# Kernel tuning notes

Measured on AMD Instinct MI355X. Metric: run time of the kernel, lower is better.

The kernel has to match this reference:

```python
import jax, jax.numpy as jnp
import numpy as np

T = 2048
D_MODEL = 4096
N_HEADS = 32
N_GROUPS = 8
HEAD_DIM = 128


def _rope_tables(tokens, head_dim, base=10000.0):
    inv_freq = 1.0 / (base ** (np.arange(0, head_dim, 2, dtype=np.float32) / head_dim))
    pos = np.arange(tokens, dtype=np.float32)
    freqs = np.einsum('t,d->td', pos, inv_freq)          # [T, D/2]
    emb = np.concatenate([freqs, freqs], axis=-1)         # [T, D]
    return jnp.asarray(np.cos(emb)), jnp.asarray(np.sin(emb))


def setup_inputs() -> dict:
    key = jax.random.key(0)
    k1, k2, k3 = jax.random.split(key, 3)
    x = jax.random.normal(k1, (T, D_MODEL), dtype=jnp.float32)
    w_qkv = jax.random.normal(k2, (D_MODEL, (N_HEADS + 2 * N_GROUPS) * HEAD_DIM), dtype=jnp.float32) * 0.02
    w_out = jax.random.normal(k3, (N_HEADS * HEAD_DIM, D_MODEL), dtype=jnp.float32) * 0.02
    cos, sin = _rope_tables(T, HEAD_DIM)
    mask = jnp.tril(jnp.ones((T, T), dtype=bool))  # causal: [suffix_tokens, total_tokens]
    return {"x": x, "w_qkv": w_qkv, "w_out": w_out, "cos": cos, "sin": sin, "mask": mask}


def _rotate_half(u):
    u1, u2 = jnp.split(u, 2, axis=-1)
    return jnp.concatenate([-u2, u1], axis=-1)


def _apply_rope(u, cos, sin):
    # u: [tokens, heads, head_dim]; cos/sin: [tokens, head_dim]
    c = cos[:, None, :]
    s = sin[:, None, :]
    return u * c + _rotate_half(u) * s


def reference(x, w_qkv, w_out, cos, sin, mask):
    group_dim = N_HEADS // N_GROUPS
    qkv = x @ w_qkv                                        # [T, (H+2G)*D]
    q, k, v = jnp.split(qkv, [N_HEADS * HEAD_DIM, (N_HEADS + N_GROUPS) * HEAD_DIM], axis=-1)
    q = q.reshape(T, N_HEADS, HEAD_DIM)
    k = k.reshape(T, N_GROUPS, HEAD_DIM)
    v = v.reshape(T, N_GROUPS, HEAD_DIM)
    q = _apply_rope(q, cos, sin)
    k = _apply_rope(k, cos, sin)
    # GQA: group queries -> [T, G, group_dim, D]
    qg = q.reshape(T, N_GROUPS, group_dim, HEAD_DIM)
    scale = 1.0 / jnp.sqrt(jnp.asarray(HEAD_DIM, dtype=q.dtype))
    scores = jnp.einsum('tghd,sgd->ghts', qg, k) * scale   # [G, gd, T, S]
    neg = jnp.asarray(jnp.finfo(scores.dtype).min, scores.dtype)
    scores = jnp.where(mask[None, None, :, :], scores, neg)
    probs = jax.nn.softmax(scores, axis=-1)
    out = jnp.einsum('ghts,sgd->tghd', probs, v)           # [T, G, gd, D]
    out = out.reshape(T, N_HEADS * HEAD_DIM)
    return out @ w_out                                     # [T, model_dim]
```

## Files before the change

kernel.cpp:

```cpp
#include <hip/hip_runtime.h>
#include <cstdint>
#include <cstddef>

#define TT   2048
#define DM   4096
#define NH   32
#define NG   8
#define HD   128
#define QKVN 6144
#define KOFF 4096
#define VOFF 5120

typedef __attribute__((ext_vector_type(8))) short bf16x8;
typedef __attribute__((ext_vector_type(4))) float f32x4;
typedef unsigned short u16;

__device__ __forceinline__ u16 f2b(float f) {
  unsigned u = __builtin_bit_cast(unsigned, f);
  u += 0x7fffu + ((u >> 16) & 1u);
  return (u16)(u >> 16);
}
__device__ __forceinline__ float b2f(u16 s) {
  unsigned u = ((unsigned)s) << 16;
  return __builtin_bit_cast(float, u);
}

__device__ __forceinline__ void gload_lds16(const void* g, void* l) {
  __builtin_amdgcn_global_load_lds(
      (const __attribute__((address_space(1))) unsigned int*)g,
      (__attribute__((address_space(3))) unsigned int*)l,
      16, 0, 0);
}

__global__ __launch_bounds__(256) void cvt_f32_bf16(
    const float* __restrict__ src, u16* __restrict__ dst, int n) {
  for (int i = (blockIdx.x * 256 + threadIdx.x) * 4; i < n; i += gridDim.x * 256 * 4) {
    float4 v = *(const float4*)(src + i);
    ushort4 o;
    o.x = f2b(v.x); o.y = f2b(v.y); o.z = f2b(v.z); o.w = f2b(v.w);
    *(ushort4*)(dst + i) = o;
  }
}

__global__ __launch_bounds__(256) void transpose_cvt(
    const float* __restrict__ src, u16* __restrict__ dst, int R, int C) {
  __shared__ u16 tile[64][66];
  const int rb = blockIdx.y * 64, cb = blockIdx.x * 64;
  const int tid = threadIdx.x;
#pragma unroll
  for (int it = 0; it < 16; ++it) {
    int idx = it * 256 + tid;
    int i = idx >> 6, j = idx & 63;
    tile[i][j] = f2b(src[(size_t)(rb + i) * C + cb + j]);
  }
  __syncthreads();
#pragma unroll
  for (int it = 0; it < 16; ++it) {
    int idx = it * 256 + tid;
    int j = idx >> 6, i = idx & 63;
    dst[(size_t)(cb + j) * R + rb + i] = tile[i][j];
  }
}

template <bool OUT_BF16>
__global__ __launch_bounds__(512) void gemm8p(
    const u16* __restrict__ A, const u16* __restrict__ Bt, void* __restrict__ Cout,
    int M, int N, int K, int nbx) {
  __shared__ __align__(16) u16 sA[2][128 * 64];
  __shared__ __align__(16) u16 sB[2][256 * 64];
  const int tid = threadIdx.x;
  const int wid = tid >> 6, lane = tid & 63;
  const int lane15 = lane & 15, laneh = lane >> 4;
  const int wm = wid >> 2, wn = wid & 3;
  const int cpx = gridDim.x >> 3;
  const int swz = ((int)blockIdx.x & 7) * cpx + ((int)blockIdx.x >> 3);
  const int m0 = (swz / nbx) * 128, n0 = (swz % nbx) * 256;
  const int xorL = (lane15 & 7) << 3;

  f32x4 acc[4][4];
#pragma unroll
  for (int m = 0; m < 4; ++m)
#pragma unroll
    for (int n = 0; n < 4; ++n)
#pragma unroll
      for (int r = 0; r < 4; ++r) acc[m][n][r] = 0.f;

  auto stageA = [&](int buf, int t) {
    const int k0 = t << 6;
#pragma unroll
    for (int i = 0; i < 2; ++i) {
      const int ebase = (wid * 2 + i) * 512;
      const int e = ebase + lane * 8;
      const int row = e >> 6;
      const int col = (e & 63) ^ ((row & 7) << 3);
      gload_lds16(A + (size_t)(m0 + row) * K + k0 + col, &sA[buf][ebase]);
    }
  };
  auto stageB = [&](int buf, int t) {
    const int k0 = t << 6;
#pragma unroll
    for (int i = 0; i < 4; ++i) {
      const int ebase = (wid * 4 + i) * 512;
      const int e = ebase + lane * 8;
      const int row = e >> 6;
      const int col = (e & 63) ^ ((row & 7) << 3);
      gload_lds16(Bt + (size_t)(n0 + row) * K + k0 + col, &sB[buf][ebase]);
    }
  };

  const int NT = K >> 6;
  stageA(0, 0);
  stageB(0, 0);
  stageA(1, 1);
  asm volatile("s_waitcnt vmcnt(2)");
  __builtin_amdgcn_s_barrier();

  for (int u = 0; u < NT; ++u) {
    const int cur = u & 1;
    bf16x8 af[4][2], bfr[4][2];
#pragma unroll
    for (int m = 0; m < 4; ++m)
#pragma unroll
      for (int ks = 0; ks < 2; ++ks)
        af[m][ks] = *(const bf16x8*)&sA[cur][(wm * 64 + m * 16 + lane15) * 64 +
                                            ((ks * 32 + laneh * 8) ^ xorL)];
#pragma unroll
    for (int n = 0; n < 2; ++n)
#pragma unroll
      for (int ks = 0; ks < 2; ++ks)
        bfr[n][ks] = *(const bf16x8*)&sB[cur][(wn * 64 + n * 16 + lane15) * 64 +
                                             ((ks * 32 + laneh * 8) ^ xorL)];
    __builtin_amdgcn_sched_barrier(0);
    if (u + 1 < NT) stageB(cur ^ 1, u + 1);
    __builtin_amdgcn_s_barrier();
    asm volatile("s_waitcnt lgkmcnt(0)");
    __builtin_amdgcn_sched_barrier(0);
    __builtin_amdgcn_s_setprio(1);
#pragma unroll
    for (int ks = 0; ks < 2; ++ks)
#pragma unroll
      for (int m = 0; m < 4; ++m)
#pragma unroll
        for (int n = 0; n < 2; ++n)
          acc[m][n] = __builtin_amdgcn_mfma_f32_16x16x32_bf16(af[m][ks], bfr[n][ks], acc[m][n], 0, 0, 0);
    __builtin_amdgcn_s_setprio(0);
    __builtin_amdgcn_s_barrier();
#pragma unroll
    for (int n = 2; n < 4; ++n)
#pragma unroll
      for (int ks = 0; ks < 2; ++ks)
        bfr[n][ks] = *(const bf16x8*)&sB[cur][(wn * 64 + n * 16 + lane15) * 64 +
                                             ((ks * 32 + laneh * 8) ^ xorL)];
    __builtin_amdgcn_sched_barrier(0);
    if (u + 2 < NT) stageA(cur, u + 2);
    __builtin_amdgcn_s_barrier();
    asm volatile("s_waitcnt lgkmcnt(0)");
    __builtin_amdgcn_sched_barrier(0);
    __builtin_amdgcn_s_setprio(1);
#pragma unroll
    for (int ks = 0; ks < 2; ++ks)
#pragma unroll
      for (int m = 0; m < 4; ++m)
#pragma unroll
        for (int n = 2; n < 4; ++n)
          acc[m][n] = __builtin_amdgcn_mfma_f32_16x16x32_bf16(af[m][ks], bfr[n][ks], acc[m][n], 0, 0, 0);
    __builtin_amdgcn_s_setprio(0);
    if (u + 2 < NT) asm volatile("s_waitcnt vmcnt(2)");
    else            asm volatile("s_waitcnt vmcnt(0)");
    __builtin_amdgcn_s_barrier();
  }
#pragma unroll
  for (int m = 0; m < 4; ++m)
#pragma unroll
    for (int n = 0; n < 4; ++n)
#pragma unroll
      for (int r = 0; r < 4; ++r) {
        const int row = m0 + wm * 64 + m * 16 + laneh * 4 + r;
        const int col = n0 + wn * 64 + n * 16 + lane15;
        const float v = acc[m][n][r];
        if (OUT_BF16) ((u16*)Cout)[(size_t)row * N + col] = f2b(v);
        else          ((float*)Cout)[(size_t)row * N + col] = v;
      }
}

__global__ __launch_bounds__(256) void rope_rearrange(
    const u16* __restrict__ qkv, const float* __restrict__ cosT,
    const float* __restrict__ sinT, u16* __restrict__ Qr, u16* __restrict__ Kr) {
  const int u = blockIdx.x * 4 + (threadIdx.x >> 6);
  const int lane = threadIdx.x & 63;
  const int t = u & (TT - 1);
  const int e = u >> 11;
  const u16* in;
  u16* outp;
  if (e < NH) {
    in = qkv + (size_t)t * QKVN + e * HD;
    outp = Qr + ((size_t)e * TT + t) * HD;
  } else {
    const int g = e - NH;
    in = qkv + (size_t)t * QKVN + KOFF + g * HD;
    outp = Kr + ((size_t)g * TT + t) * HD;
  }
  const float u1 = b2f(in[lane]), u2 = b2f(in[lane + 64]);
  const float c1 = cosT[t * HD + lane], s1 = sinT[t * HD + lane];
  const float c2 = cosT[t * HD + lane + 64], s2 = sinT[t * HD + lane + 64];
  outp[lane]      = f2b(u1 * c1 - u2 * s1);
  outp[lane + 64] = f2b(u2 * c2 + u1 * s2);
}

__global__ __launch_bounds__(256) void vtrans(
    const u16* __restrict__ qkv, u16* __restrict__ VT) {
  __shared__ u16 tile[64][66];
  const int g = blockIdx.z;
  const int t0 = blockIdx.x * 64, d0 = blockIdx.y * 64;
  const int tid = threadIdx.x;
#pragma unroll
  for (int it = 0; it < 16; ++it) {
    int idx = it * 256 + tid;
    int i = idx >> 6, j = idx & 63;
    tile[i][j] = qkv[(size_t)(t0 + i) * QKVN + VOFF + g * HD + d0 + j];
  }
  __syncthreads();
#pragma unroll
  for (int it = 0; it < 16; ++it) {
    int idx = it * 256 + tid;
    int j = idx >> 6, i = idx & 63;
    VT[((size_t)g * HD + d0 + j) * TT + t0 + i] = tile[i][j];
  }
}

__global__ __launch_bounds__(512) void attn(
    const u16* __restrict__ Qr, const u16* __restrict__ Kr,
    const u16* __restrict__ VT, u16* __restrict__ AO) {
  __shared__ __align__(16) u16 sK[128 * 128];
  __shared__ __align__(16) u16 sV[128 * 128];
  const int bid = blockIdx.x;
  const int swz = (bid & 7) * 32 + (bid >> 3);
  const int h = swz >> 3, p = swz & 7;
  const int g = h >> 2;
  const int tid = threadIdx.x, wid = tid >> 6, lane = tid & 63;
  const int lane15 = lane & 15, laneh = lane >> 4;
  const int xorL = (lane15 & 7) << 3;
  const u16* Qh = Qr + (size_t)h * TT * HD;
  const u16* Kg = Kr + (size_t)g * TT * HD;
  const u16* Vg = VT + (size_t)g * HD * TT;
  const float scale = 0.08838834764831845f;

  for (int pass = 0; pass < 2; ++pass) {
    const int qt = pass ? (15 - p) : p;
    bf16x8 qf[4];
    const int qrow0 = qt * 128 + wid * 16;
#pragma unroll
    for (int ks = 0; ks < 4; ++ks)
      qf[ks] = *(const bf16x8*)(Qh + (size_t)(qrow0 + lane15) * HD + ks * 32 + laneh * 8);

    f32x4 acc_o[8];
    float mrow[4], lrow[4];
#pragma unroll
    for (int n = 0; n < 8; ++n)
#pragma unroll
      for (int r = 0; r < 4; ++r) acc_o[n][r] = 0.f;
#pragma unroll
    for (int r = 0; r < 4; ++r) { mrow[r] = -1e30f; lrow[r] = 0.f; }

    for (int kv = 0; kv <= qt; ++kv) {
#pragma unroll
      for (int i = 0; i < 4; ++i) {
        const int ebase = (wid * 4 + i) * 512;
        const int e = ebase + lane * 8;
        const int row = e >> 7;
        const int col = (e & 127) ^ ((row & 7) << 3);
        gload_lds16(Kg + (size_t)(kv * 128 + row) * HD + col, &sK[ebase]);
        gload_lds16(Vg + (size_t)row * TT + kv * 128 + col, &sV[ebase]);
      }
      __syncthreads();

      f32x4 s[8];
#pragma unroll
      for (int n = 0; n < 8; ++n)
#pragma unroll
        for (int r = 0; r < 4; ++r) s[n][r] = 0.f;
      __builtin_amdgcn_s_setprio(1);
#pragma unroll
      for (int ks = 0; ks < 4; ++ks) {
        bf16x8 kf[8];
#pragma unroll
        for (int n = 0; n < 8; ++n)
          kf[n] = *(const bf16x8*)&sK[(n * 16 + lane15) * 128 + ((ks * 32 + laneh * 8) ^ xorL)];
#pragma unroll
        for (int n = 0; n < 8; ++n)
          s[n] = __builtin_amdgcn_mfma_f32_16x16x32_bf16(qf[ks], kf[n], s[n], 0, 0, 0);
      }
      __builtin_amdgcn_s_setprio(0);
      __syncthreads();

      if (kv == qt) {
#pragma unroll
        for (int n = 0; n < 8; ++n)
#pragma unroll
          for (int r = 0; r < 4; ++r) {
            const int ql = wid * 16 + laneh * 4 + r;
            const int sl = n * 16 + lane15;
            s[n][r] = (sl > ql) ? -1e30f : s[n][r] * scale;
          }
      } else {
#pragma unroll
        for (int n = 0; n < 8; ++n)
#pragma unroll
          for (int r = 0; r < 4; ++r) s[n][r] *= scale;
      }
#pragma unroll
      for (int r = 0; r < 4; ++r) {
        float pm = s[0][r];
#pragma unroll
        for (int n = 1; n < 8; ++n) pm = fmaxf(pm, s[n][r]);
        pm = fmaxf(pm, __shfl_xor(pm, 1));
        pm = fmaxf(pm, __shfl_xor(pm, 2));
        pm = fmaxf(pm, __shfl_xor(pm, 4));
        pm = fmaxf(pm, __shfl_xor(pm, 8));
        const float mnew = fmaxf(mrow[r], pm);
        const float corr = __expf(mrow[r] - mnew);
        mrow[r] = mnew;
        float ps = 0.f;
#pragma unroll
        for (int n = 0; n < 8; ++n) {
          const float pr = __expf(s[n][r] - mnew);
          s[n][r] = pr;
          ps += pr;
        }
        ps += __shfl_xor(ps, 1); ps += __shfl_xor(ps, 2);
        ps += __shfl_xor(ps, 4); ps += __shfl_xor(ps, 8);
        lrow[r] = lrow[r] * corr + ps;
#pragma unroll
        for (int n = 0; n < 8; ++n) acc_o[n][r] *= corr;
      }
#pragma unroll
      for (int n = 0; n < 8; ++n)
#pragma unroll
        for (int r = 0; r < 4; ++r) {
          const int prow = wid * 16 + laneh * 4 + r;
          const int pcol = (n * 16 + lane15) ^ (((laneh * 4 + r) & 7) << 3);
          sK[prow * 128 + pcol] = f2b(s[n][r]);
        }
      __builtin_amdgcn_s_setprio(1);
#pragma unroll
      for (int ks = 0; ks < 4; ++ks) {
        bf16x8 pf, vf[8];
        pf = *(const bf16x8*)&sK[(wid * 16 + lane15) * 128 + ((ks * 32 + laneh * 8) ^ xorL)];
#pragma unroll
        for (int n = 0; n < 8; ++n)
          vf[n] = *(const bf16x8*)&sV[(n * 16 + lane15) * 128 + ((ks * 32 + laneh * 8) ^ xorL)];
#pragma unroll
        for (int n = 0; n < 8; ++n)
          acc_o[n] = __builtin_amdgcn_mfma_f32_16x16x32_bf16(pf, vf[n], acc_o[n], 0, 0, 0);
      }
      __builtin_amdgcn_s_setprio(0);
      __syncthreads();
    }
    float inv[4];
#pragma unroll
    for (int r = 0; r < 4; ++r) inv[r] = 1.f / lrow[r];
#pragma unroll
    for (int n = 0; n < 8; ++n)
#pragma unroll
      for (int r = 0; r < 4; ++r) {
        const int trow = qt * 128 + wid * 16 + laneh * 4 + r;
        AO[(size_t)trow * DM + h * HD + n * 16 + lane15] = f2b(acc_o[n][r] * inv[r]);
      }
  }
}

extern "C" void kernel_launch(void* const* d_in, const int* in_sizes, int n_in,
                              void* d_out, int out_size, void* d_ws, size_t ws_size,
                              hipStream_t stream) {
  const float* x     = (const float*)d_in[0];
  const float* w_qkv = (const float*)d_in[1];
  const float* w_out = (const float*)d_in[2];
  const float* cosT  = (const float*)d_in[3];
  const float* sinT  = (const float*)d_in[4];
  float* out = (float*)d_out;

  char* ws = (char*)d_ws;
  u16* wT  = (u16*)(ws);
  u16* xb  = (u16*)(ws + 50331648);
  u16* qkv = (u16*)(ws + 50331648 + 16777216);
  u16* Qr  = (u16*)(ws + 50331648 + 16777216 + 25165824);
  u16* Kr  = Qr + (size_t)NH * TT * HD;
  u16* VT  = Kr + (size_t)NG * TT * HD;
  u16* AO  = xb;

  cvt_f32_bf16<<<2048, 256, 0, stream>>>(x, xb, TT * DM);
  transpose_cvt<<<dim3(QKVN / 64, DM / 64), 256, 0, stream>>>(w_qkv, wT, DM, QKVN);
  gemm8p<true><<<dim3((TT / 128) * (QKVN / 256)), 512, 0, stream>>>(
      xb, wT, qkv, TT, QKVN, DM, QKVN / 256);
  rope_rearrange<<<(TT * (NH + NG)) / 4, 256, 0, stream>>>(qkv, cosT, sinT, Qr, Kr);
  vtrans<<<dim3(TT / 64, HD / 64, NG), 256, 0, stream>>>(qkv, VT);
  transpose_cvt<<<dim3(DM / 64, DM / 64), 256, 0, stream>>>(w_out, wT, DM, DM);
  attn<<<NH * 8, 512, 0, stream>>>(Qr, Kr, VT, AO);
  gemm8p<false><<<dim3((TT / 128) * (DM / 256)), 512, 0, stream>>>(
      AO, wT, out, TT, DM, DM, DM / 256);
}
```

Measured before the change: 372.1 us.

## Double-buffer K/V loads in attention and widen QKV GEMM tile to 384 columns

The attention kernel now double-buffers K and V tiles in shared memory, prefetching the next KV block while computing the current one. P is staged in a per-warp buffer instead of reusing sK, which drops one block-wide barrier per iteration. The GEMM is templated on its N-tile width, and the QKV projection uses 384-column tiles, giving 256 blocks instead of 384 and more B reuse per block. The cost is more shared memory per attention block (about 160KB) and more accumulator registers in the GEMM, which may limit occupancy.

New measurement: 329.5 us. 11.5% less time.

```diff
diff --git a/kernel.cpp b/kernel.cpp
--- a/kernel.cpp
+++ b/kernel.cpp
@@ -62,26 +62,26 @@
   }
 }
 
-template <bool OUT_BF16>
+template <int WN, bool OUT_BF16>
 __global__ __launch_bounds__(512) void gemm8p(
     const u16* __restrict__ A, const u16* __restrict__ Bt, void* __restrict__ Cout,
     int M, int N, int K, int nbx) {
   __shared__ __align__(16) u16 sA[2][128 * 64];
-  __shared__ __align__(16) u16 sB[2][256 * 64];
+  __shared__ __align__(16) u16 sB[2][WN * 64 * 64];
   const int tid = threadIdx.x;
   const int wid = tid >> 6, lane = tid & 63;
   const int lane15 = lane & 15, laneh = lane >> 4;
   const int wm = wid >> 2, wn = wid & 3;
   const int cpx = gridDim.x >> 3;
   const int swz = ((int)blockIdx.x & 7) * cpx + ((int)blockIdx.x >> 3);
-  const int m0 = (swz / nbx) * 128, n0 = (swz % nbx) * 256;
+  const int m0 = (swz / nbx) * 128, n0 = (swz % nbx) * (WN * 64);
   const int xorL = (lane15 & 7) << 3;
 
-  f32x4 acc[4][4];
+  f32x4 acc[4][WN];
 #pragma unroll
   for (int m = 0; m < 4; ++m)
 #pragma unroll
-    for (int n = 0; n < 4; ++n)
+    for (int n = 0; n < WN; ++n)
 #pragma unroll
       for (int r = 0; r < 4; ++r) acc[m][n][r] = 0.f;
 
@@ -99,8 +99,8 @@
   auto stageB = [&](int buf, int t) {
     const int k0 = t << 6;
 #pragma unroll
-    for (int i = 0; i < 4; ++i) {
-      const int ebase = (wid * 4 + i) * 512;
+    for (int i = 0; i < WN; ++i) {
+      const int ebase = (wid * WN + i) * 512;
       const int e = ebase + lane * 8;
       const int row = e >> 6;
       const int col = (e & 63) ^ ((row & 7) << 3);
@@ -117,7 +117,7 @@
 
   for (int u = 0; u < NT; ++u) {
     const int cur = u & 1;
-    bf16x8 af[4][2], bfr[4][2];
+    bf16x8 af[4][2], bfr[WN][2];
 #pragma unroll
     for (int m = 0; m < 4; ++m)
 #pragma unroll
@@ -125,10 +125,10 @@
         af[m][ks] = *(const bf16x8*)&sA[cur][(wm * 64 + m * 16 + lane15) * 64 +
                                             ((ks * 32 + laneh * 8) ^ xorL)];
 #pragma unroll
-    for (int n = 0; n < 2; ++n)
+    for (int n = 0; n < WN / 2; ++n)
 #pragma unroll
       for (int ks = 0; ks < 2; ++ks)
-        bfr[n][ks] = *(const bf16x8*)&sB[cur][(wn * 64 + n * 16 + lane15) * 64 +
+        bfr[n][ks] = *(const bf16x8*)&sB[cur][(wn * (WN * 16) + n * 16 + lane15) * 64 +
                                              ((ks * 32 + laneh * 8) ^ xorL)];
     __builtin_amdgcn_sched_barrier(0);
     if (u + 1 < NT) stageB(cur ^ 1, u + 1);
@@ -141,15 +141,15 @@
 #pragma unroll
       for (int m = 0; m < 4; ++m)
 #pragma unroll
-        for (int n = 0; n < 2; ++n)
+        for (int n = 0; n < WN / 2; ++n)
           acc[m][n] = __builtin_amdgcn_mfma_f32_16x16x32_bf16(af[m][ks], bfr[n][ks], acc[m][n], 0, 0, 0);
     __builtin_amdgcn_s_setprio(0);
     __builtin_amdgcn_s_barrier();
 #pragma unroll
-    for (int n = 2; n < 4; ++n)
+    for (int n = WN / 2; n < WN; ++n)
 #pragma unroll
       for (int ks = 0; ks < 2; ++ks)
-        bfr[n][ks] = *(const bf16x8*)&sB[cur][(wn * 64 + n * 16 + lane15) * 64 +
+        bfr[n][ks] = *(const bf16x8*)&sB[cur][(wn * (WN * 16) + n * 16 + lane15) * 64 +
                                              ((ks * 32 + laneh * 8) ^ xorL)];
     __builtin_amdgcn_sched_barrier(0);
     if (u + 2 < NT) stageA(cur, u + 2);
@@ -162,7 +162,7 @@
 #pragma unroll
       for (int m = 0; m < 4; ++m)
 #pragma unroll
-        for (int n = 2; n < 4; ++n)
+        for (int n = WN / 2; n < WN; ++n)
           acc[m][n] = __builtin_amdgcn_mfma_f32_16x16x32_bf16(af[m][ks], bfr[n][ks], acc[m][n], 0, 0, 0);
     __builtin_amdgcn_s_setprio(0);
     if (u + 2 < NT) asm volatile("s_waitcnt vmcnt(2)");
@@ -172,11 +172,11 @@
 #pragma unroll
   for (int m = 0; m < 4; ++m)
 #pragma unroll
-    for (int n = 0; n < 4; ++n)
+    for (int n = 0; n < WN; ++n)
 #pragma unroll
       for (int r = 0; r < 4; ++r) {
         const int row = m0 + wm * 64 + m * 16 + laneh * 4 + r;
-        const int col = n0 + wn * 64 + n * 16 + lane15;
+        const int col = n0 + wn * (WN * 16) + n * 16 + lane15;
         const float v = acc[m][n][r];
         if (OUT_BF16) ((u16*)Cout)[(size_t)row * N + col] = f2b(v);
         else          ((float*)Cout)[(size_t)row * N + col] = v;
@@ -231,8 +231,9 @@
 __global__ __launch_bounds__(512) void attn(
     const u16* __restrict__ Qr, const u16* __restrict__ Kr,
     const u16* __restrict__ VT, u16* __restrict__ AO) {
-  __shared__ __align__(16) u16 sK[128 * 128];
-  __shared__ __align__(16) u16 sV[128 * 128];
+  __shared__ __align__(16) u16 sK[2][128 * 128];
+  __shared__ __align__(16) u16 sV[2][128 * 128];
+  __shared__ __align__(16) u16 sP[8][16 * 128];
   const int bid = blockIdx.x;
   const int swz = (bid & 7) * 32 + (bid >> 3);
   const int h = swz >> 3, p = swz & 7;
@@ -245,6 +246,18 @@
   const u16* Vg = VT + (size_t)g * HD * TT;
   const float scale = 0.08838834764831845f;
 
+  auto stageKV = [&](int buf, int kv) {
+#pragma unroll
+    for (int i = 0; i < 4; ++i) {
+      const int ebase = (wid * 4 + i) * 512;
+      const int e = ebase + lane * 8;
+      const int row = e >> 7;
+      const int col = (e & 127) ^ ((row & 7) << 3);
+      gload_lds16(Kg + (size_t)(kv * 128 + row) * HD + col, &sK[buf][ebase]);
+      gload_lds16(Vg + (size_t)row * TT + kv * 128 + col, &sV[buf][ebase]);
+    }
+  };
+
   for (int pass = 0; pass < 2; ++pass) {
     const int qt = pass ? (15 - p) : p;
     bf16x8 qf[4];
@@ -262,17 +275,14 @@
 #pragma unroll
     for (int r = 0; r < 4; ++r) { mrow[r] = -1e30f; lrow[r] = 0.f; }
 
+    stageKV(0, 0);
     for (int kv = 0; kv <= qt; ++kv) {
-#pragma unroll
-      for (int i = 0; i < 4; ++i) {
-        const int ebase = (wid * 4 + i) * 512;
-        const int e = ebase + lane * 8;
-        const int row = e >> 7;
-        const int col = (e & 127) ^ ((row & 7) << 3);
-        gload_lds16(Kg + (size_t)(kv * 128 + row) * HD + col, &sK[ebase]);
-        gload_lds16(Vg + (size_t)row * TT + kv * 128 + col, &sV[ebase]);
-      }
-      __syncthreads();
+      const int cur = kv & 1;
+      if (kv < qt) stageKV(cur ^ 1, kv + 1);
+      __builtin_amdgcn_sched_barrier(0);
+      if (kv < qt) asm volatile("s_waitcnt vmcnt(8)");
+      else         asm volatile("s_waitcnt vmcnt(0)");
+      __builtin_amdgcn_s_barrier();
 
       f32x4 s[8];
 #pragma unroll
@@ -285,13 +295,12 @@
         bf16x8 kf[8];
 #pragma unroll
         for (int n = 0; n < 8; ++n)
-          kf[n] = *(const bf16x8*)&sK[(n * 16 + lane15) * 128 + ((ks * 32 + laneh * 8) ^ xorL)];
+          kf[n] = *(const bf16x8*)&sK[cur][(n * 16 + lane15) * 128 + ((ks * 32 + laneh * 8) ^ xorL)];
 #pragma unroll
         for (int n = 0; n < 8; ++n)
           s[n] = __builtin_amdgcn_mfma_f32_16x16x32_bf16(qf[ks], kf[n], s[n], 0, 0, 0);
       }
       __builtin_amdgcn_s_setprio(0);
-      __syncthreads();
 
       if (kv == qt) {
 #pragma unroll
@@ -337,24 +346,24 @@
       for (int n = 0; n < 8; ++n)
 #pragma unroll
         for (int r = 0; r < 4; ++r) {
-          const int prow = wid * 16 + laneh * 4 + r;
-          const int pcol = (n * 16 + lane15) ^ (((laneh * 4 + r) & 7) << 3);
-          sK[prow * 128 + pcol] = f2b(s[n][r]);
+          const int prow = laneh * 4 + r;
+          const int pcol = (n * 16 + lane15) ^ ((prow & 7) << 3);
+          sP[wid][prow * 128 + pcol] = f2b(s[n][r]);
         }
       __builtin_amdgcn_s_setprio(1);
 #pragma unroll
       for (int ks = 0; ks < 4; ++ks) {
         bf16x8 pf, vf[8];
-        pf = *(const bf16x8*)&sK[(wid * 16 + lane15) * 128 + ((ks * 32 + laneh * 8) ^ xorL)];
-#pragma unroll
-        for (int n = 0; n < 8; ++n)
-          vf[n] = *(const bf16x8*)&sV[(n * 16 + lane15) * 128 + ((ks * 32 + laneh * 8) ^ xorL)];
+        pf = *(const bf16x8*)&sP[wid][lane15 * 128 + ((ks * 32 + laneh * 8) ^ xorL)];
+#pragma unroll
+        for (int n = 0; n < 8; ++n)
+          vf[n] = *(const bf16x8*)&sV[cur][(n * 16 + lane15) * 128 + ((ks * 32 + laneh * 8) ^ xorL)];
 #pragma unroll
         for (int n = 0; n < 8; ++n)
           acc_o[n] = __builtin_amdgcn_mfma_f32_16x16x32_bf16(pf, vf[n], acc_o[n], 0, 0, 0);
       }
       __builtin_amdgcn_s_setprio(0);
-      __syncthreads();
+      __builtin_amdgcn_s_barrier();
     }
     float inv[4];
 #pragma unroll
@@ -390,12 +399,12 @@
 
   cvt_f32_bf16<<<2048, 256, 0, stream>>>(x, xb, TT * DM);
   transpose_cvt<<<dim3(QKVN / 64, DM / 64), 256, 0, stream>>>(w_qkv, wT, DM, QKVN);
-  gemm8p<true><<<dim3((TT / 128) * (QKVN / 256)), 512, 0, stream>>>(
-      xb, wT, qkv, TT, QKVN, DM, QKVN / 256);
+  gemm8p<6, true><<<dim3((TT / 128) * (QKVN / 384)), 512, 0, stream>>>(
+      xb, wT, qkv, TT, QKVN, DM, QKVN / 384);
   rope_rearrange<<<(TT * (NH + NG)) / 4, 256, 0, stream>>>(qkv, cosT, sinT, Qr, Kr);
   vtrans<<<dim3(TT / 64, HD / 64, NG), 256, 0, stream>>>(qkv, VT);
   transpose_cvt<<<dim3(DM / 64, DM / 64), 256, 0, stream>>>(w_out, wT, DM, DM);
   attn<<<NH * 8, 512, 0, stream>>>(Qr, Kr, VT, AO);
-  gemm8p<false><<<dim3((TT / 128) * (DM / 256)), 512, 0, stream>>>(
+  gemm8p<4, false><<<dim3((TT / 128) * (DM / 256)), 512, 0, stream>>>(
       AO, wT, out, TT, DM, DM, DM / 256);
 }
```
